# Kernel tuning notes

Hardware: AMD Instinct MI355X
Metric: run time of the kernel (lower is better)

## Reference

```python
import jax, jax.numpy as jnp
import numpy as np

EPS = 1e-12  # matches NTMNet epsilon


def setup_inputs() -> dict:
    key = jax.random.key(0)
    ks = jax.random.split(key, 12)
    B, L, C, D, H = 64, 16384, 64, 256, 100
    F = D + 1 * C  # inputs concat flattened reading (1 reader)
    def w(k, shape):
        return jax.random.normal(k, shape, dtype=jnp.float32) * 0.05
    return {
        "inputs": w(ks[0], (B, D)),
        "reading": w(ks[1], (B, 1, C)),
        "memory": w(ks[2], (B, L, C)),
        "W1": w(ks[3], (F, H)), "b1": jnp.zeros((H,), jnp.float32),
        "W2": w(ks[4], (H, H)), "b2": jnp.zeros((H,), jnp.float32),
        "Wk_r": w(ks[5], (H, C)), "bk_r": jnp.zeros((C,), jnp.float32),
        "Ws_r": w(ks[6], (H, 1)), "bs_r": jnp.zeros((1,), jnp.float32),
        "Wk_w": w(ks[7], (H, C)), "bk_w": jnp.zeros((C,), jnp.float32),
        "Ws_w": w(ks[8], (H, 1)), "bs_w": jnp.zeros((1,), jnp.float32),
        "We": w(ks[9], (H, C)), "be": jnp.zeros((C,), jnp.float32),
        "Wa": w(ks[10], (H, C)), "ba": jnp.zeros((C,), jnp.float32),
    }


def reference(inputs, reading, memory, W1, b1, W2, b2,
              Wk_r, bk_r, Ws_r, bs_r, Wk_w, bk_w, Ws_w, bs_w,
              We, be, Wa, ba):
    B = inputs.shape[0]
    feat = jnp.concatenate([inputs, reading.reshape(B, -1)], axis=-1)
    h = jnp.tanh(jnp.tanh(feat @ W1 + b1) @ W2 + b2)  # [B,H]

    # memory normalized over the whole (lines, cols) matrix per batch element
    mnorm = jnp.sqrt(jnp.sum(memory * memory, axis=(-2, -1), keepdims=True))
    mem_n = memory / jnp.maximum(mnorm, EPS)  # [B,L,C]

    def addressing(Wk, bk, Ws, bs):
        # content addressing: cosine-sim of key vs memory rows, sharpened softmax
        kvec = h @ Wk + bk  # [B,C] (no activation)
        kvec = kvec / jnp.maximum(jnp.linalg.norm(kvec, axis=1, keepdims=True), EPS)
        s = jax.nn.sigmoid(h @ Ws + bs)  # [B,1] strength
        K = jnp.einsum('blc,bc->bl', mem_n, kvec)  # [B,L]
        return jax.nn.softmax(K * s, axis=-1)  # [B,L]

    # read head
    w_r = addressing(Wk_r, bk_r, Ws_r, bs_r)
    read = jnp.einsum('bl,blc->bc', w_r, memory)  # [B,C]

    # write head: erase then add
    w_w = addressing(Wk_w, bk_w, Ws_w, bs_w)
    e = jax.nn.sigmoid(h @ We + be)  # [B,C]
    a = jax.nn.sigmoid(h @ Wa + ba)  # [B,C]
    ww = w_w[:, :, None]  # [B,L,1]
    new_mem = memory * (1.0 - ww * e[:, None, :]) + ww * a[:, None, :]  # [B,L,C]
    return read, new_mem
```

## Files before the change

kernel.cpp:

```cpp
#include <hip/hip_runtime.h>
#include <math.h>

#define B 64
#define L 16384
#define C 64
#define D 256
#define H 100
#define F 320
#define EPSV 1e-12f

__device__ inline float waveReduceSum(float v) {
    v += __shfl_xor(v, 32);
    v += __shfl_xor(v, 16);
    v += __shfl_xor(v, 8);
    v += __shfl_xor(v, 4);
    v += __shfl_xor(v, 2);
    v += __shfl_xor(v, 1);
    return v;
}

__global__ __launch_bounds__(128) void head_kernel(
    const float* __restrict__ inputs, const float* __restrict__ reading,
    const float* __restrict__ W1, const float* __restrict__ b1,
    const float* __restrict__ W2, const float* __restrict__ b2,
    const float* __restrict__ Wk_r, const float* __restrict__ bk_r,
    const float* __restrict__ Ws_r, const float* __restrict__ bs_r,
    const float* __restrict__ Wk_w, const float* __restrict__ bk_w,
    const float* __restrict__ Ws_w, const float* __restrict__ bs_w,
    const float* __restrict__ We, const float* __restrict__ be,
    const float* __restrict__ Wa, const float* __restrict__ ba,
    float* __restrict__ kv_r, float* __restrict__ kv_w,
    float* __restrict__ ev, float* __restrict__ av,
    float* __restrict__ s_r, float* __restrict__ s_w)
{
    const int b = blockIdx.x;
    const int t = threadIdx.x;
    __shared__ float feat[F];
    __shared__ float h1[H];
    __shared__ float h2[H];
    __shared__ float kr[C], kw[C], ee[C], aa[C];
    __shared__ float inv_r, inv_w;

    for (int i = t; i < D; i += 128) feat[i] = inputs[b * D + i];
    if (t < C) feat[D + t] = reading[b * C + t];
    __syncthreads();

    if (t < H) {
        float acc = b1[t];
        for (int f = 0; f < F; ++f) acc += feat[f] * W1[f * H + t];
        h1[t] = tanhf(acc);
    }
    __syncthreads();
    if (t < H) {
        float acc = b2[t];
        for (int k = 0; k < H; ++k) acc += h1[k] * W2[k * H + t];
        h2[t] = tanhf(acc);
    }
    __syncthreads();

    if (t < C) {
        float a0 = bk_r[t], a1 = bk_w[t], a2 = be[t], a3 = ba[t];
        for (int j = 0; j < H; ++j) {
            float hv = h2[j];
            a0 += hv * Wk_r[j * C + t];
            a1 += hv * Wk_w[j * C + t];
            a2 += hv * We[j * C + t];
            a3 += hv * Wa[j * C + t];
        }
        kr[t] = a0; kw[t] = a1;
        ee[t] = 1.f / (1.f + expf(-a2));
        aa[t] = 1.f / (1.f + expf(-a3));
    } else if (t == 64 || t == 65) {
        const float* Ws = (t == 64) ? Ws_r : Ws_w;
        float acc = (t == 64) ? bs_r[0] : bs_w[0];
        for (int j = 0; j < H; ++j) acc += h2[j] * Ws[j];
        float s = 1.f / (1.f + expf(-acc));
        if (t == 64) s_r[b] = s; else s_w[b] = s;
    }
    __syncthreads();
    if (t == 0) {
        float nr = 0.f, nw = 0.f;
        for (int c = 0; c < C; ++c) { nr += kr[c] * kr[c]; nw += kw[c] * kw[c]; }
        inv_r = 1.f / fmaxf(sqrtf(nr), EPSV);
        inv_w = 1.f / fmaxf(sqrtf(nw), EPSV);
    }
    __syncthreads();
    if (t < C) {
        kv_r[b * C + t] = kr[t] * inv_r;
        kv_w[b * C + t] = kw[t] * inv_w;
        ev[b * C + t] = ee[t];
        av[b * C + t] = aa[t];
    }
}

__global__ __launch_bounds__(256) void passA_kernel(
    const float* __restrict__ mem,
    const float* __restrict__ kv_r, const float* __restrict__ kv_w,
    float* __restrict__ dot_r, float* __restrict__ dot_w,
    float* __restrict__ sumsq)
{
    const int b = blockIdx.y;
    const int t = threadIdx.x;
    const int wave = t >> 6, lane = t & 63;
    const int sub = lane >> 4, m = lane & 15;

    const float4 kr = *(const float4*)(kv_r + b * C + m * 4);
    const float4 kw = *(const float4*)(kv_w + b * C + m * 4);
    const float4* memv = (const float4*)(mem + (size_t)b * L * C);

    float lss = 0.f;
    const int row0 = blockIdx.x * 512;
    #pragma unroll 2
    for (int it = 0; it < 32; ++it) {
        const int row = row0 + it * 16 + wave * 4 + sub;
        const float4 v = memv[row * 16 + m];
        float pr = v.x * kr.x + v.y * kr.y + v.z * kr.z + v.w * kr.w;
        float pw = v.x * kw.x + v.y * kw.y + v.z * kw.z + v.w * kw.w;
        lss += v.x * v.x + v.y * v.y + v.z * v.z + v.w * v.w;
        pr += __shfl_xor(pr, 1); pr += __shfl_xor(pr, 2);
        pr += __shfl_xor(pr, 4); pr += __shfl_xor(pr, 8);
        pw += __shfl_xor(pw, 1); pw += __shfl_xor(pw, 2);
        pw += __shfl_xor(pw, 4); pw += __shfl_xor(pw, 8);
        if (m == 0) {
            dot_r[b * L + row] = pr;
            dot_w[b * L + row] = pw;
        }
    }
    lss = waveReduceSum(lss);
    __shared__ float wsum[4];
    if (lane == 0) wsum[wave] = lss;
    __syncthreads();
    if (t == 0) atomicAdd(&sumsq[b], wsum[0] + wsum[1] + wsum[2] + wsum[3]);
}

__global__ __launch_bounds__(256) void softmax_kernel(
    float* __restrict__ dot_r, float* __restrict__ dot_w,
    const float* __restrict__ s_r, const float* __restrict__ s_w,
    const float* __restrict__ sumsq)
{
    const int b = blockIdx.x;
    float* p = (blockIdx.y == 0 ? dot_r : dot_w) + (size_t)b * L;
    const float sv = (blockIdx.y == 0 ? s_r : s_w)[b];
    const float scale = sv / fmaxf(sqrtf(sumsq[b]), EPSV);
    const int t = threadIdx.x;
    const int wave = t >> 6, lane = t & 63;
    __shared__ float sm[4];
    __shared__ float bmax_s, bsum_s;

    float lmax = -INFINITY;
    for (int i = t; i < L; i += 256) lmax = fmaxf(lmax, p[i] * scale);
    for (int off = 32; off; off >>= 1) lmax = fmaxf(lmax, __shfl_xor(lmax, off));
    if (lane == 0) sm[wave] = lmax;
    __syncthreads();
    if (t == 0) bmax_s = fmaxf(fmaxf(sm[0], sm[1]), fmaxf(sm[2], sm[3]));
    __syncthreads();
    const float bmax = bmax_s;

    float lsum = 0.f;
    for (int i = t; i < L; i += 256) lsum += expf(p[i] * scale - bmax);
    lsum = waveReduceSum(lsum);
    if (lane == 0) sm[wave] = lsum;
    __syncthreads();
    if (t == 0) bsum_s = sm[0] + sm[1] + sm[2] + sm[3];
    __syncthreads();
    const float inv = 1.f / bsum_s;

    for (int i = t; i < L; i += 256) p[i] = expf(p[i] * scale - bmax) * inv;
}

__global__ __launch_bounds__(256) void passB_kernel(
    const float* __restrict__ mem,
    const float* __restrict__ w_r, const float* __restrict__ w_w,
    const float* __restrict__ ev, const float* __restrict__ av,
    float* __restrict__ out_read, float* __restrict__ new_mem)
{
    const int b = blockIdx.y;
    const int t = threadIdx.x;
    const int wave = t >> 6, lane = t & 63;
    const int sub = lane >> 4, m = lane & 15;

    const float4 e4 = *(const float4*)(ev + b * C + m * 4);
    const float4 a4 = *(const float4*)(av + b * C + m * 4);
    const float4* memv = (const float4*)(mem + (size_t)b * L * C);
    float4* outv = (float4*)(new_mem + (size_t)b * L * C);

    float4 racc = {0.f, 0.f, 0.f, 0.f};
    const int row0 = blockIdx.x * 512;
    #pragma unroll 2
    for (int it = 0; it < 32; ++it) {
        const int row = row0 + it * 16 + wave * 4 + sub;
        const float wr = w_r[b * L + row];
        const float ww = w_w[b * L + row];
        const float4 v = memv[row * 16 + m];
        float4 nm;
        nm.x = v.x * (1.f - ww * e4.x) + ww * a4.x;
        nm.y = v.y * (1.f - ww * e4.y) + ww * a4.y;
        nm.z = v.z * (1.f - ww * e4.z) + ww * a4.z;
        nm.w = v.w * (1.f - ww * e4.w) + ww * a4.w;
        outv[row * 16 + m] = nm;
        racc.x += wr * v.x; racc.y += wr * v.y;
        racc.z += wr * v.z; racc.w += wr * v.w;
    }
    racc.x += __shfl_xor(racc.x, 16); racc.x += __shfl_xor(racc.x, 32);
    racc.y += __shfl_xor(racc.y, 16); racc.y += __shfl_xor(racc.y, 32);
    racc.z += __shfl_xor(racc.z, 16); racc.z += __shfl_xor(racc.z, 32);
    racc.w += __shfl_xor(racc.w, 16); racc.w += __shfl_xor(racc.w, 32);
    __shared__ float lds[4][64];
    if (lane < 16) {
        lds[wave][m * 4 + 0] = racc.x;
        lds[wave][m * 4 + 1] = racc.y;
        lds[wave][m * 4 + 2] = racc.z;
        lds[wave][m * 4 + 3] = racc.w;
    }
    __syncthreads();
    if (t < 64) {
        float tot = lds[0][t] + lds[1][t] + lds[2][t] + lds[3][t];
        atomicAdd(&out_read[b * C + t], tot);
    }
}

extern "C" void kernel_launch(void* const* d_in, const int* in_sizes, int n_in,
                              void* d_out, int out_size, void* d_ws, size_t ws_size,
                              hipStream_t stream) {
    const float* inputs  = (const float*)d_in[0];
    const float* reading = (const float*)d_in[1];
    const float* memory  = (const float*)d_in[2];
    const float* W1 = (const float*)d_in[3];
    const float* b1 = (const float*)d_in[4];
    const float* W2 = (const float*)d_in[5];
    const float* b2 = (const float*)d_in[6];
    const float* Wk_r = (const float*)d_in[7];
    const float* bk_r = (const float*)d_in[8];
    const float* Ws_r = (const float*)d_in[9];
    const float* bs_r = (const float*)d_in[10];
    const float* Wk_w = (const float*)d_in[11];
    const float* bk_w = (const float*)d_in[12];
    const float* Ws_w = (const float*)d_in[13];
    const float* bs_w = (const float*)d_in[14];
    const float* We = (const float*)d_in[15];
    const float* be = (const float*)d_in[16];
    const float* Wa = (const float*)d_in[17];
    const float* ba = (const float*)d_in[18];

    float* ws = (float*)d_ws;
    float* kv_r  = ws;
    float* kv_w  = ws + 4096;
    float* ev    = ws + 8192;
    float* av    = ws + 12288;
    float* s_r   = ws + 16384;
    float* s_w   = ws + 16448;
    float* sumsq = ws + 16512;
    float* dot_r = ws + 16576;
    float* dot_w = dot_r + (size_t)B * L;

    float* out = (float*)d_out;
    float* out_read = out;
    float* new_mem  = out + 4096;

    hipMemsetAsync(sumsq, 0, B * sizeof(float), stream);
    hipMemsetAsync(out_read, 0, B * C * sizeof(float), stream);

    head_kernel<<<B, 128, 0, stream>>>(
        inputs, reading, W1, b1, W2, b2, Wk_r, bk_r, Ws_r, bs_r,
        Wk_w, bk_w, Ws_w, bs_w, We, be, Wa, ba,
        kv_r, kv_w, ev, av, s_r, s_w);

    passA_kernel<<<dim3(32, B), 256, 0, stream>>>(
        memory, kv_r, kv_w, dot_r, dot_w, sumsq);

    softmax_kernel<<<dim3(B, 2), 256, 0, stream>>>(
        dot_r, dot_w, s_r, s_w, sumsq);

    passB_kernel<<<dim3(32, B), 256, 0, stream>>>(
        memory, dot_r, dot_w, ev, av, out_read, new_mem);
}
```

Measured before the change: 597.3 us.

## Interleave read/write dots and defer softmax normalization into the update pass

Pass A now writes the read and write dot products interleaved as float2 and packs the two shuffle reductions into one shared chain. The softmax kernel becomes a stats-only kernel, one 1024-thread block per batch holding all values in registers, and emits scale, max and inverse sum. Pass B recomputes the attention weights with expf from those stats, which removes the softmax writeback and second read of the weight arrays. Pass B also uses nontemporal stores for the large new_mem output, and the head kernel's key norm becomes a wave reduction. The cost is extra exp work in pass B and higher register pressure in the stats kernel.

```diff
diff --git a/kernel.cpp b/kernel.cpp
--- a/kernel.cpp
+++ b/kernel.cpp
@@ -8,6 +8,8 @@
 #define H 100
 #define F 320
 #define EPSV 1e-12f
+
+typedef float nfloat4 __attribute__((ext_vector_type(4)));
 
 __device__ inline float waveReduceSum(float v) {
     v += __shfl_xor(v, 32);
@@ -78,11 +80,14 @@
         if (t == 64) s_r[b] = s; else s_w[b] = s;
     }
     __syncthreads();
-    if (t == 0) {
-        float nr = 0.f, nw = 0.f;
-        for (int c = 0; c < C; ++c) { nr += kr[c] * kr[c]; nw += kw[c] * kw[c]; }
-        inv_r = 1.f / fmaxf(sqrtf(nr), EPSV);
-        inv_w = 1.f / fmaxf(sqrtf(nw), EPSV);
+    if (t < 64) {
+        const float xr = kr[t], xw = kw[t];
+        const float nr = waveReduceSum(xr * xr);
+        const float nw = waveReduceSum(xw * xw);
+        if (t == 0) {
+            inv_r = 1.f / fmaxf(sqrtf(nr), EPSV);
+            inv_w = 1.f / fmaxf(sqrtf(nw), EPSV);
+        }
     }
     __syncthreads();
     if (t < C) {
@@ -96,7 +101,7 @@
 __global__ __launch_bounds__(256) void passA_kernel(
     const float* __restrict__ mem,
     const float* __restrict__ kv_r, const float* __restrict__ kv_w,
-    float* __restrict__ dot_r, float* __restrict__ dot_w,
+    float2* __restrict__ dot2,
     float* __restrict__ sumsq)
 {
     const int b = blockIdx.y;
@@ -107,24 +112,25 @@
     const float4 kr = *(const float4*)(kv_r + b * C + m * 4);
     const float4 kw = *(const float4*)(kv_w + b * C + m * 4);
     const float4* memv = (const float4*)(mem + (size_t)b * L * C);
+    float2* d2 = dot2 + (size_t)b * L;
 
     float lss = 0.f;
     const int row0 = blockIdx.x * 512;
-    #pragma unroll 2
+    #pragma unroll 4
     for (int it = 0; it < 32; ++it) {
         const int row = row0 + it * 16 + wave * 4 + sub;
         const float4 v = memv[row * 16 + m];
         float pr = v.x * kr.x + v.y * kr.y + v.z * kr.z + v.w * kr.w;
         float pw = v.x * kw.x + v.y * kw.y + v.z * kw.z + v.w * kw.w;
         lss += v.x * v.x + v.y * v.y + v.z * v.z + v.w * v.w;
-        pr += __shfl_xor(pr, 1); pr += __shfl_xor(pr, 2);
-        pr += __shfl_xor(pr, 4); pr += __shfl_xor(pr, 8);
-        pw += __shfl_xor(pw, 1); pw += __shfl_xor(pw, 2);
-        pw += __shfl_xor(pw, 4); pw += __shfl_xor(pw, 8);
-        if (m == 0) {
-            dot_r[b * L + row] = pr;
-            dot_w[b * L + row] = pw;
-        }
+        pr += __shfl_xor(pr, 1);
+        pw += __shfl_xor(pw, 1);
+        float x = (m & 1) ? pw : pr;
+        x += __shfl_xor(x, 2);
+        x += __shfl_xor(x, 4);
+        x += __shfl_xor(x, 8);
+        const float y = __shfl_xor(x, 1);
+        if (m == 0) d2[row] = make_float2(x, y);
     }
     lss = waveReduceSum(lss);
     __shared__ float wsum[4];
@@ -133,44 +139,70 @@
     if (t == 0) atomicAdd(&sumsq[b], wsum[0] + wsum[1] + wsum[2] + wsum[3]);
 }
 
-__global__ __launch_bounds__(256) void softmax_kernel(
-    float* __restrict__ dot_r, float* __restrict__ dot_w,
+__global__ __launch_bounds__(1024) void stats_kernel(
+    const float2* __restrict__ dot2,
     const float* __restrict__ s_r, const float* __restrict__ s_w,
-    const float* __restrict__ sumsq)
+    const float* __restrict__ sumsq,
+    float* __restrict__ stats)
 {
     const int b = blockIdx.x;
-    float* p = (blockIdx.y == 0 ? dot_r : dot_w) + (size_t)b * L;
-    const float sv = (blockIdx.y == 0 ? s_r : s_w)[b];
-    const float scale = sv / fmaxf(sqrtf(sumsq[b]), EPSV);
     const int t = threadIdx.x;
     const int wave = t >> 6, lane = t & 63;
-    __shared__ float sm[4];
-    __shared__ float bmax_s, bsum_s;
-
-    float lmax = -INFINITY;
-    for (int i = t; i < L; i += 256) lmax = fmaxf(lmax, p[i] * scale);
-    for (int off = 32; off; off >>= 1) lmax = fmaxf(lmax, __shfl_xor(lmax, off));
-    if (lane == 0) sm[wave] = lmax;
-    __syncthreads();
-    if (t == 0) bmax_s = fmaxf(fmaxf(sm[0], sm[1]), fmaxf(sm[2], sm[3]));
-    __syncthreads();
-    const float bmax = bmax_s;
-
-    float lsum = 0.f;
-    for (int i = t; i < L; i += 256) lsum += expf(p[i] * scale - bmax);
-    lsum = waveReduceSum(lsum);
-    if (lane == 0) sm[wave] = lsum;
-    __syncthreads();
-    if (t == 0) bsum_s = sm[0] + sm[1] + sm[2] + sm[3];
-    __syncthreads();
-    const float inv = 1.f / bsum_s;
-
-    for (int i = t; i < L; i += 256) p[i] = expf(p[i] * scale - bmax) * inv;
+    const float invn = 1.f / fmaxf(sqrtf(sumsq[b]), EPSV);
+    const float sc_r = s_r[b] * invn;
+    const float sc_w = s_w[b] * invn;
+    const float2* p = dot2 + (size_t)b * L;
+
+    float2 v[16];
+    #pragma unroll
+    for (int k = 0; k < 16; ++k) v[k] = p[t + k * 1024];
+
+    float mr = -INFINITY, mw = -INFINITY;
+    #pragma unroll
+    for (int k = 0; k < 16; ++k) {
+        mr = fmaxf(mr, v[k].x * sc_r);
+        mw = fmaxf(mw, v[k].y * sc_w);
+    }
+    #pragma unroll
+    for (int off = 32; off; off >>= 1) {
+        mr = fmaxf(mr, __shfl_xor(mr, off));
+        mw = fmaxf(mw, __shfl_xor(mw, off));
+    }
+    __shared__ float redr[16], redw[16];
+    if (lane == 0) { redr[wave] = mr; redw[wave] = mw; }
+    __syncthreads();
+    if (t == 0) {
+        float a = redr[0], c = redw[0];
+        for (int i = 1; i < 16; ++i) { a = fmaxf(a, redr[i]); c = fmaxf(c, redw[i]); }
+        redr[0] = a; redw[0] = c;
+    }
+    __syncthreads();
+    const float bmr = redr[0], bmw = redw[0];
+    __syncthreads();
+
+    float sr = 0.f, sw = 0.f;
+    #pragma unroll
+    for (int k = 0; k < 16; ++k) {
+        sr += expf(v[k].x * sc_r - bmr);
+        sw += expf(v[k].y * sc_w - bmw);
+    }
+    sr = waveReduceSum(sr);
+    sw = waveReduceSum(sw);
+    if (lane == 0) { redr[wave] = sr; redw[wave] = sw; }
+    __syncthreads();
+    if (t == 0) {
+        float a = 0.f, c = 0.f;
+        for (int i = 0; i < 16; ++i) { a += redr[i]; c += redw[i]; }
+        float* st = stats + b * 8;
+        st[0] = sc_r; st[1] = bmr; st[2] = 1.f / a;
+        st[3] = sc_w; st[4] = bmw; st[5] = 1.f / c;
+    }
 }
 
 __global__ __launch_bounds__(256) void passB_kernel(
     const float* __restrict__ mem,
-    const float* __restrict__ w_r, const float* __restrict__ w_w,
+    const float2* __restrict__ dot2,
+    const float* __restrict__ stats,
     const float* __restrict__ ev, const float* __restrict__ av,
     float* __restrict__ out_read, float* __restrict__ new_mem)
 {
@@ -181,23 +213,28 @@
 
     const float4 e4 = *(const float4*)(ev + b * C + m * 4);
     const float4 a4 = *(const float4*)(av + b * C + m * 4);
+    const float* st = stats + b * 8;
+    const float sc_r = st[0], mx_r = st[1], inv_r = st[2];
+    const float sc_w = st[3], mx_w = st[4], inv_w = st[5];
     const float4* memv = (const float4*)(mem + (size_t)b * L * C);
-    float4* outv = (float4*)(new_mem + (size_t)b * L * C);
+    nfloat4* outv = (nfloat4*)(new_mem + (size_t)b * L * C);
+    const float2* d2 = dot2 + (size_t)b * L;
 
     float4 racc = {0.f, 0.f, 0.f, 0.f};
     const int row0 = blockIdx.x * 512;
     #pragma unroll 2
     for (int it = 0; it < 32; ++it) {
         const int row = row0 + it * 16 + wave * 4 + sub;
-        const float wr = w_r[b * L + row];
-        const float ww = w_w[b * L + row];
+        const float2 d = d2[row];
+        const float wr = expf(d.x * sc_r - mx_r) * inv_r;
+        const float ww = expf(d.y * sc_w - mx_w) * inv_w;
         const float4 v = memv[row * 16 + m];
-        float4 nm;
+        nfloat4 nm;
         nm.x = v.x * (1.f - ww * e4.x) + ww * a4.x;
         nm.y = v.y * (1.f - ww * e4.y) + ww * a4.y;
         nm.z = v.z * (1.f - ww * e4.z) + ww * a4.z;
         nm.w = v.w * (1.f - ww * e4.w) + ww * a4.w;
-        outv[row * 16 + m] = nm;
+        __builtin_nontemporal_store(nm, &outv[row * 16 + m]);
         racc.x += wr * v.x; racc.y += wr * v.y;
         racc.z += wr * v.z; racc.w += wr * v.w;
     }
@@ -250,8 +287,8 @@
     float* s_r   = ws + 16384;
     float* s_w   = ws + 16448;
     float* sumsq = ws + 16512;
-    float* dot_r = ws + 16576;
-    float* dot_w = dot_r + (size_t)B * L;
+    float* stats = ws + 16576;
+    float* dot2f = ws + 17408;
 
     float* out = (float*)d_out;
     float* out_read = out;
@@ -266,11 +303,11 @@
         kv_r, kv_w, ev, av, s_r, s_w);
 
     passA_kernel<<<dim3(32, B), 256, 0, stream>>>(
-        memory, kv_r, kv_w, dot_r, dot_w, sumsq);
-
-    softmax_kernel<<<dim3(B, 2), 256, 0, stream>>>(
-        dot_r, dot_w, s_r, s_w, sumsq);
+        memory, kv_r, kv_w, (float2*)dot2f, sumsq);
+
+    stats_kernel<<<B, 1024, 0, stream>>>(
+        (const float2*)dot2f, s_r, s_w, sumsq, stats);
 
     passB_kernel<<<dim3(32, B), 256, 0, stream>>>(
-        memory, dot_r, dot_w, ev, av, out_read, new_mem);
-}
+        memory, (const float2*)dot2f, stats, ev, av, out_read, new_mem);
+}
```

Measured after the change: 570.7 us. -4.5%, faster.
